# Kernel tuning notes

Measured on AMD Instinct MI355X. Metric: run time of the kernel, lower is better.

## Reference

```python
import jax, jax.numpy as jnp
import numpy as np

N, F, E, A, H = 50000, 64, 1600000, 8, 16
RECEPTIVE_FIELD = 7


def setup_inputs() -> dict:
    key = jax.random.key(0)
    ks = jax.random.split(key, 12)
    inp = {
        "x": jax.random.normal(ks[0], (N, F), dtype=jnp.float32),
        "edge_index": jax.random.randint(ks[1], (2, E), 0, N, dtype=jnp.int64),
        "w1": jax.random.normal(ks[2], (F, H), dtype=jnp.float32) * 0.1,
        "b1": jax.random.normal(ks[3], (H,), dtype=jnp.float32) * 0.1,
        "w2": jax.random.normal(ks[4], (H, H), dtype=jnp.float32) * 0.1,
        "b2": jax.random.normal(ks[5], (H,), dtype=jnp.float32) * 0.1,
        "w3": jax.random.normal(ks[6], (H, F), dtype=jnp.float32) * 0.1,
        "b3": jax.random.normal(ks[7], (F,), dtype=jnp.float32) * 0.1,
        "fc1_w": jax.random.normal(ks[8], ((1 + RECEPTIVE_FIELD) * F, F), dtype=jnp.float32) * 0.05,
        "fc1_b": jax.random.normal(ks[9], (F,), dtype=jnp.float32) * 0.05,
        "fc2_w": jax.random.normal(ks[10], (F, A), dtype=jnp.float32) * 0.1,
        "fc2_b": jax.random.normal(ks[11], (A,), dtype=jnp.float32) * 0.1,
    }
    return inp


def _mlp(x, w1, b1, w2, b2, w3, b3):
    h = jax.nn.relu(x @ w1 + b1)
    h = jax.nn.relu(h @ w2 + b2)
    return h @ w3 + b3


def _agg_mean(x, src, dst):
    # scatter-mean: mean of source-node features over incoming edges per target
    s = jax.ops.segment_sum(x[src], dst, num_segments=N)          # [N, F]
    cnt = jax.ops.segment_sum(jnp.ones((src.shape[0], 1), x.dtype), dst, num_segments=N)
    return s / jnp.maximum(cnt, 1.0)  # nodes with no in-edges -> 0 (torch mean aggr)


def reference(x, edge_index, w1, b1, w2, b2, w3, b3, fc1_w, fc1_b, fc2_w, fc2_b):
    src, dst = edge_index[0], edge_index[1]
    mlp = lambda t: _mlp(t, w1, b1, w2, b2, w3, b3)
    fields = [mlp(mlp(x))]
    for i in range(RECEPTIVE_FIELD):
        x_ = mlp(x)
        for _ in range(i + 1):
            x_ = _agg_mean(x_, src, dst)
        fields.append(mlp(x_))
    f = jnp.concatenate(fields, axis=1)          # [N, 8*F]
    h = f @ fc1_w + fc1_b                        # [N, F]
    logits = h @ fc2_w + fc2_b                   # [N, A]
    return jax.nn.softmax(logits, axis=-1)       # Categorical probs
```

## Files before the change

### kernel.cpp

```cpp
#include <hip/hip_runtime.h>
#include <hip/hip_fp16.h>


#define NB2MAX 400
#define NBLK   256
#define CAP2   32
#define CAPC   48
#define CAPB   6144
#define OVCAP  1024
#define LCAP   6144
#define CAPN   64

__global__ __launch_bounds__(1024) void binfill_k(
    const int* __restrict__ src, const int* __restrict__ dst, int E, int n,
    int* __restrict__ gcur, int* __restrict__ ovbuf,
    int* __restrict__ bins, int* __restrict__ cnts,
    const float* __restrict__ w1, const float* __restrict__ w3,
    const float* __restrict__ b3, const float* __restrict__ fc1w,
    const float* __restrict__ fc1b, const float* __restrict__ fc2w,
    const float* __restrict__ fc2b,
    float* __restrict__ M, float* __restrict__ cvec,
    float* __restrict__ W31, float* __restrict__ c31) {
    __shared__ int lbuf[NB2MAX * CAP2];
    __shared__ int lcnt[NB2MAX];
    __shared__ int lflush[NB2MAX];
    int tid = threadIdx.x;
    int NB = (n + 127) >> 7;

    if ((int)blockIdx.x >= NBLK) {
        float* fl = (float*)lbuf;
        int s = (int)blockIdx.x - NBLK;
        if (s == 0) {
            if (tid < 256) {
                int i = tid >> 4, j = tid & 15;
                float a = 0.f;
                for (int g = 0; g < 64; g++) a += w3[i * 64 + g] * w1[g * 16 + j];
                W31[tid] = a;
            } else if (tid < 272) {
                int j = tid - 256;
                float a = 0.f;
                for (int g = 0; g < 64; g++) a += b3[g] * w1[g * 16 + j];
                c31[j] = a;
            } else if (tid >= 320 && tid < 384) {
                int h = tid - 320;
                float a = 0.f;
                for (int r = 0; r < 512; r++) a += b3[r & 63] * fc1w[r * 64 + h];
                fl[h] = a;
            }
            __syncthreads();
            if (tid < 8) {
                float a = fc2b[tid];
                for (int h = 0; h < 64; h++) a += (fc1b[h] + fl[h]) * fc2w[h * 8 + tid];
                cvec[tid] = a;
            }
        } else {
            int k = s - 1;
            {
                int i = tid >> 6, h = tid & 63;
                float a = 0.f;
                const float* f1 = fc1w + (size_t)(k * 64) * 64 + h;
                for (int g = 0; g < 64; g++) a += w3[i * 64 + g] * f1[g * 64];
                fl[i * 64 + h] = a;
            }
            __syncthreads();
            if (tid < 128) {
                int i = tid >> 3, j = tid & 7;
                float a = 0.f;
                for (int h = 0; h < 64; h++) a += fl[i * 64 + h] * fc2w[h * 8 + j];
                M[k * 128 + i * 8 + j] = a;
            }
        }
        return;
    }

    for (int b = tid; b < NB; b += 1024) { lcnt[b] = 0; lflush[b] = 0; }
    __syncthreads();
    int blk = blockIdx.x;
    int chunk = (E + NBLK - 1) / NBLK;
    int beg = blk * chunk;
    int end = beg + chunk; if (end > E) end = E;
    for (int t0 = beg; t0 < end; t0 += 1024) {
        int e = t0 + tid;
        if (e < end) {
            int d = dst[e], s = src[e];
            if ((unsigned)d < (unsigned)n && (unsigned)s < (unsigned)n) {
                int b = d >> 7;
                int pk = ((d & 127) << 16) | s;
                int pos = atomicAdd(&lcnt[b], 1);
                if (pos < CAP2) lbuf[b * CAP2 + pos] = pk;
                else {
                    int p = atomicAdd(&gcur[b], 1);
                    if (p < OVCAP) ovbuf[b * OVCAP + p] = pk;
                }
            }
        }
        __syncthreads();
        for (int b = tid; b < NB; b += 1024) {
            int cnt = lcnt[b]; if (cnt > CAP2) cnt = CAP2;
            int fl2 = lflush[b];
            size_t cell = ((size_t)b * NBLK + blk) * CAPC;
            int base = 0;
            while (cnt - base >= 16) {
                if (fl2 + 16 <= CAPC) {
                    int* dp = bins + cell + fl2;
                    #pragma unroll
                    for (int q = 0; q < 16; q++) dp[q] = lbuf[b * CAP2 + base + q];
                    fl2 += 16;
                } else {
                    int p = atomicAdd(&gcur[b], 16);
                    for (int q = 0; q < 16; q++)
                        if (p + q < OVCAP) ovbuf[b * OVCAP + p + q] = lbuf[b * CAP2 + base + q];
                }
                base += 16;
            }
            int rem = cnt - base;
            if (base > 0)
                for (int q = 0; q < rem; q++) lbuf[b * CAP2 + q] = lbuf[b * CAP2 + base + q];
            lcnt[b] = rem; lflush[b] = fl2;
        }
        __syncthreads();
    }
    for (int b = tid; b < NB; b += 1024) {
        int cnt = lcnt[b]; if (cnt > CAP2) cnt = CAP2;
        int fl2 = lflush[b];
        size_t cell = ((size_t)b * NBLK + blk) * CAPC;
        if (fl2 + cnt <= CAPC) {
            for (int q = 0; q < cnt; q++) bins[cell + fl2 + q] = lbuf[b * CAP2 + q];
            fl2 += cnt;
        } else {
            int p = atomicAdd(&gcur[b], cnt);
            for (int q = 0; q < cnt; q++)
                if (p + q < OVCAP) ovbuf[b * OVCAP + p + q] = lbuf[b * CAP2 + q];
        }
        cnts[(size_t)blk * NB + b] = fl2;
    }
}

__global__ __launch_bounds__(256) void csr2_k(
    const int* __restrict__ bins, const int* __restrict__ cnts,
    const int* __restrict__ gcur, const int* __restrict__ ovbuf,
    unsigned short* __restrict__ csrp_s, int2* __restrict__ nd_s,
    int* __restrict__ csr, int2* __restrict__ be, int* __restrict__ lcnt3,
    int n) {
    __shared__ int hist[128], pref[128], cur[128], slot[128];
    __shared__ int scnt[NBLK];
    __shared__ int lbuf[LCAP];
    __shared__ int sov;
    __shared__ int ccnt[3], cbase[3];
    int tid = threadIdx.x;
    int NB = (n + 127) >> 7;
    int b = blockIdx.x;
    if (tid < 128) { hist[tid] = 0; cur[tid] = 0; }
    if (tid < 3) ccnt[tid] = 0;
    scnt[tid] = cnts[(size_t)tid * NB + b];
    if (tid == 0) {
        int g = gcur[b];
        sov = g < 0 ? 0 : (g > OVCAP ? OVCAP : g);
    }
    __syncthreads();
    {
        int c = scnt[tid];
        size_t cell = ((size_t)b * NBLK + tid) * CAPC;
        for (int i = 0; i < c; i++) atomicAdd(&hist[bins[cell + i] >> 16], 1);
    }
    if (tid == 0)
        for (int i = 0; i < sov; i++) atomicAdd(&hist[ovbuf[b * OVCAP + i] >> 16], 1);
    __syncthreads();
    if (tid == 0) {
        int r = 0;
        for (int i = 0; i < 128; i++) { pref[i] = r; r += hist[i]; }
    }
    __syncthreads();
    {
        int c = scnt[tid];
        size_t cell = ((size_t)b * NBLK + tid) * CAPC;
        for (int i = 0; i < c; i++) {
            int pk = bins[cell + i];
            int dl = pk >> 16;
            int pos = pref[dl] + atomicAdd(&cur[dl], 1);
            if (pos < LCAP) lbuf[pos] = pk & 0xffff;
        }
    }
    if (tid == 0) {
        for (int i = 0; i < sov; i++) {
            int pk = ovbuf[b * OVCAP + i];
            int dl = pk >> 16;
            int pos = pref[dl] + atomicAdd(&cur[dl], 1);
            if (pos < LCAP) lbuf[pos] = pk & 0xffff;
        }
    }
    __syncthreads();
    int myc = -1, lpos = 0;
    if (tid < 128) {
        int d = (b << 7) + tid;
        if (d < n) {
            int cnt = hist[tid];
            myc = cnt <= 32 ? 0 : (cnt <= 48 ? 1 : 2);
            lpos = atomicAdd(&ccnt[myc], 1);
        }
    }
    __syncthreads();
    if (tid < 3) cbase[tid] = atomicAdd(&lcnt3[tid], ccnt[tid]);
    __syncthreads();
    if (myc >= 0) {
        int d = (b << 7) + tid;
        int cnt = hist[tid];
        int s = myc * n + cbase[myc] + lpos;
        slot[tid] = s;
        nd_s[s] = make_int2(d, cnt);
        if (cnt > CAPN) {
            int s0 = b * CAPB + pref[tid];
            be[d] = make_int2(s0 + CAPN, s0 + cnt);
            for (int j = CAPN; j < cnt; j++)
                csr[s0 + j] = lbuf[pref[tid] + j] << 2;
        }
    }
    __syncthreads();
    for (int q = tid; q < 128 * CAPN; q += 256) {
        int dl = q >> 6, j = q & 63;
        int d = (b << 7) + dl;
        if (d >= n) break;
        int cnt = hist[dl];
        int v = (j < cnt) ? lbuf[pref[dl] + j] : n;
        int pos = ((j & 3) << 4) | (j >> 2);
        csrp_s[(size_t)slot[dl] * CAPN + pos] = (unsigned short)v;
    }
}

__device__ __forceinline__ void acc_row(uint2 u, float& ax, float& ay,
                                        float& az, float& aw) {
    __half2 p = *reinterpret_cast<const __half2*>(&u.x);
    __half2 q = *reinterpret_cast<const __half2*>(&u.y);
    float2 f = __half22float2(p), g = __half22float2(q);
    ax += f.x; ay += f.y; az += g.x; aw += g.y;
}

__global__ __launch_bounds__(256, 4) void proj_k(
    const float* __restrict__ x, __half* __restrict__ z0, __half* __restrict__ z1,
    float* __restrict__ logits,
    const float* __restrict__ w1, const float* __restrict__ b1,
    const float* __restrict__ w2, const float* __restrict__ b2,
    const float* __restrict__ W31, const float* __restrict__ c31,
    const float* __restrict__ M0, const float* __restrict__ cvec, int n) {
    __shared__ float sx[16 * 68];
    __shared__ float sw1[1024], sw2[256], sW[256], sM[128];
    __shared__ float sb1[16], sb2[16], sc[16], scv[8];
    int tid = threadIdx.x;
    for (int i = tid; i < 1024; i += 256) sw1[i] = w1[i];
    sw2[tid] = w2[tid];
    sW[tid] = W31[tid];
    if (tid < 128) sM[tid] = M0[tid];
    if (tid < 16) { sb1[tid] = b1[tid]; sb2[tid] = b2[tid]; sc[tid] = c31[tid]; }
    if (tid < 8) scv[tid] = cvec[tid];
    if (blockIdx.x == 0 && tid < 16) {
        ((unsigned short*)z0)[(size_t)n * 16 + tid] = 0;
        ((unsigned short*)z1)[(size_t)n * 16 + tid] = 0;
    }
    int node0 = blockIdx.x * 16;
    {
        int r = tid >> 4, c4 = tid & 15;
        if (node0 + r < n) {
            float4 v = ((const float4*)(x + (size_t)(node0 + r) * 64))[c4];
            float* dstp = sx + r * 68 + c4 * 4;
            dstp[0] = v.x; dstp[1] = v.y; dstp[2] = v.z; dstp[3] = v.w;
        }
    }
    __syncthreads();
    int nl = tid >> 4, jj = tid & 15;
    int node = node0 + nl;
    if (node >= n) return;
    float t1 = 0.f;
    const float* xr = sx + nl * 68;
    #pragma unroll
    for (int g = 0; g < 64; g++) t1 += xr[g] * sw1[g * 16 + jj];
    t1 = fmaxf(t1 + sb1[jj], 0.f);
    float t2 = sb2[jj];
    #pragma unroll
    for (int i = 0; i < 16; i++) t2 += __shfl(t1, i, 16) * sw2[i * 16 + jj];
    t2 = fmaxf(t2, 0.f);
    float zv = sc[jj];
    #pragma unroll
    for (int i = 0; i < 16; i++) zv += __shfl(t2, i, 16) * sW[i * 16 + jj];
    z0[(size_t)node * 16 + jj] = __float2half(zv);
    float hv = fmaxf(zv + sb1[jj], 0.f);
    float f2 = sb2[jj];
    #pragma unroll
    for (int i = 0; i < 16; i++) f2 += __shfl(hv, i, 16) * sw2[i * 16 + jj];
    f2 = fmaxf(f2, 0.f);
    float p0 = f2 * sM[jj * 8 + 0], p1 = f2 * sM[jj * 8 + 1];
    float p2 = f2 * sM[jj * 8 + 2], p3 = f2 * sM[jj * 8 + 3];
    float p4 = f2 * sM[jj * 8 + 4], p5 = f2 * sM[jj * 8 + 5];
    float p6 = f2 * sM[jj * 8 + 6], p7 = f2 * sM[jj * 8 + 7];
    #pragma unroll
    for (int off = 1; off < 16; off <<= 1) {
        p0 += __shfl_xor(p0, off, 16); p1 += __shfl_xor(p1, off, 16);
        p2 += __shfl_xor(p2, off, 16); p3 += __shfl_xor(p3, off, 16);
        p4 += __shfl_xor(p4, off, 16); p5 += __shfl_xor(p5, off, 16);
        p6 += __shfl_xor(p6, off, 16); p7 += __shfl_xor(p7, off, 16);
    }
    if (jj < 8) {
        float myp = jj == 0 ? p0 : jj == 1 ? p1 : jj == 2 ? p2 : jj == 3 ? p3
                  : jj == 4 ? p4 : jj == 5 ? p5 : jj == 6 ? p6 : p7;
        logits[(size_t)node * 8 + jj] = scv[jj] + myp;
    }
}

__global__ __launch_bounds__(256, 4) void hop_k(
    const __half* __restrict__ zin, __half* __restrict__ zout,
    float* __restrict__ logits,
    const unsigned short* __restrict__ csrp_s, const int2* __restrict__ nd_s,
    const int2* __restrict__ be, const int* __restrict__ csr,
    const int* __restrict__ lcnt3,
    const float* __restrict__ w2, const float* __restrict__ b1,
    const float* __restrict__ b2, const float* __restrict__ M, int n, int FB) {
    __shared__ float sw2[256], sM[128], sb1[16], sb2[16];
    int tid = threadIdx.x;
    if ((int)blockIdx.x < FB) {
        sw2[tid] = w2[tid];
        if (tid < 128) sM[tid] = M[tid];
        if (tid < 16) { sb1[tid] = b1[tid]; sb2[tid] = b2[tid]; }
        __syncthreads();
        int nid = blockIdx.x * 256 + tid;
        if (nid >= n) return;
        float h[16];
        const __half2* zp = (const __half2*)(zin + (size_t)nid * 16);
        #pragma unroll
        for (int q = 0; q < 8; q++) {
            float2 f = __half22float2(zp[q]);
            h[2 * q] = f.x; h[2 * q + 1] = f.y;
        }
        #pragma unroll
        for (int i = 0; i < 16; i++) h[i] = fmaxf(h[i] + sb1[i], 0.f);
        float t2[16];
        #pragma unroll
        for (int j = 0; j < 16; j++) {
            float a = sb2[j];
            #pragma unroll
            for (int i = 0; i < 16; i++) a += h[i] * sw2[i * 16 + j];
            t2[j] = fmaxf(a, 0.f);
        }
        float* lp = logits + (size_t)nid * 8;
        #pragma unroll
        for (int j = 0; j < 8; j++) {
            float l = 0.f;
            #pragma unroll
            for (int i = 0; i < 16; i++) l += t2[i] * sM[i * 8 + j];
            lp[j] += l;
        }
        return;
    }
    int wave = tid >> 6;
    int lane = tid & 63;
    int quarter = lane >> 4;
    int l16 = lane & 15;
    int t4 = l16 >> 2, ch = l16 & 3;
    int idx = (((int)blockIdx.x - FB) * 4 + wave) * 4 + quarter;
    if (idx >= n) return;
    int ns = lcnt3[0], nm = lcnt3[1];
    int tier; size_t row;
    if (idx < ns)           { tier = 0; row = (size_t)idx; }
    else if (idx < ns + nm) { tier = 1; row = (size_t)n + (idx - ns); }
    else                    { tier = 2; row = 2 * (size_t)n + (idx - ns - nm); }
    int2 nd = nd_s[row];
    int node = nd.x, degi = nd.y;
    const uint4* ip = (const uint4*)(csrp_s + (row << 6));
    uint4 pa = ip[t4 * 2];
    int r0 = pa.x & 0xffff, r1 = pa.x >> 16;
    int r2 = pa.y & 0xffff, r3 = pa.y >> 16;
    int r4 = pa.z & 0xffff, r5 = pa.z >> 16;
    int r6 = pa.w & 0xffff, r7 = pa.w >> 16;
    const uint2* z2 = (const uint2*)zin;
    uint2 u0 = z2[((size_t)r0 << 2) + ch];
    uint2 u1 = z2[((size_t)r1 << 2) + ch];
    uint2 u2 = z2[((size_t)r2 << 2) + ch];
    uint2 u3 = z2[((size_t)r3 << 2) + ch];
    uint2 u4 = z2[((size_t)r4 << 2) + ch];
    uint2 u5 = z2[((size_t)r5 << 2) + ch];
    uint2 u6 = z2[((size_t)r6 << 2) + ch];
    uint2 u7 = z2[((size_t)r7 << 2) + ch];
    float ax = 0.f, ay = 0.f, az = 0.f, aw = 0.f;
    acc_row(u0, ax, ay, az, aw); acc_row(u1, ax, ay, az, aw);
    acc_row(u2, ax, ay, az, aw); acc_row(u3, ax, ay, az, aw);
    acc_row(u4, ax, ay, az, aw); acc_row(u5, ax, ay, az, aw);
    acc_row(u6, ax, ay, az, aw); acc_row(u7, ax, ay, az, aw);
    if (tier >= 1) {
        uint4 pb = ip[t4 * 2 + 1];
        int r8 = pb.x & 0xffff, r9 = pb.x >> 16;
        int rA = pb.y & 0xffff, rB = pb.y >> 16;
        uint2 u8 = z2[((size_t)r8 << 2) + ch];
        uint2 u9 = z2[((size_t)r9 << 2) + ch];
        uint2 uA = z2[((size_t)rA << 2) + ch];
        uint2 uB = z2[((size_t)rB << 2) + ch];
        acc_row(u8, ax, ay, az, aw); acc_row(u9, ax, ay, az, aw);
        acc_row(uA, ax, ay, az, aw); acc_row(uB, ax, ay, az, aw);
        if (tier == 2) {
            int rC = pb.z & 0xffff, rD = pb.z >> 16;
            int rE = pb.w & 0xffff, rF = pb.w >> 16;
            uint2 uC = z2[((size_t)rC << 2) + ch];
            uint2 uD = z2[((size_t)rD << 2) + ch];
            uint2 uE = z2[((size_t)rE << 2) + ch];
            uint2 uF = z2[((size_t)rF << 2) + ch];
            acc_row(uC, ax, ay, az, aw); acc_row(uD, ax, ay, az, aw);
            acc_row(uE, ax, ay, az, aw); acc_row(uF, ax, ay, az, aw);
            if (degi > CAPN) {
                int2 r = be[node];
                for (int q = r.x + t4; q < r.y; q += 4) {
                    uint2 u = z2[(size_t)csr[q] + ch];
                    acc_row(u, ax, ay, az, aw);
                }
            }
        }
    }
    #pragma unroll
    for (int off = 8; off >= 4; off >>= 1) {
        ax += __shfl_down(ax, off, 16);
        ay += __shfl_down(ay, off, 16);
        az += __shfl_down(az, off, 16);
        aw += __shfl_down(aw, off, 16);
    }
    if (l16 < 4) {
        float inv = 1.f / (float)(degi > 0 ? degi : 1);
        __half2 h01 = __floats2half2_rn(ax * inv, ay * inv);
        __half2 h23 = __floats2half2_rn(az * inv, aw * inv);
        uint2 w;
        w.x = *reinterpret_cast<unsigned int*>(&h01);
        w.y = *reinterpret_cast<unsigned int*>(&h23);
        ((uint2*)(zout + (size_t)node * 16))[l16] = w;
    }
}

__global__ __launch_bounds__(256) void fieldsoft_k(
    const __half* __restrict__ z, float* __restrict__ logits,
    const float* __restrict__ w2, const float* __restrict__ b1,
    const float* __restrict__ b2, const float* __restrict__ M, int n) {
    __shared__ float sw2[256], sM[128], sb1[16], sb2[16];
    int tid = threadIdx.x;
    sw2[tid] = w2[tid];
    if (tid < 128) sM[tid] = M[tid];
    if (tid < 16) { sb1[tid] = b1[tid]; sb2[tid] = b2[tid]; }
    __syncthreads();
    int nid = blockIdx.x * 256 + tid;
    if (nid >= n) return;
    float h[16];
    const __half2* zp = (const __half2*)(z + (size_t)nid * 16);
    #pragma unroll
    for (int q = 0; q < 8; q++) {
        float2 f = __half22float2(zp[q]);
        h[2 * q] = f.x; h[2 * q + 1] = f.y;
    }
    #pragma unroll
    for (int i = 0; i < 16; i++) h[i] = fmaxf(h[i] + sb1[i], 0.f);
    float t2[16];
    #pragma unroll
    for (int j = 0; j < 16; j++) {
        float a = sb2[j];
        #pragma unroll
        for (int i = 0; i < 16; i++) a += h[i] * sw2[i * 16 + j];
        t2[j] = fmaxf(a, 0.f);
    }
    float4* lp4 = (float4*)(logits + (size_t)nid * 8);
    float4 l0 = lp4[0], l1 = lp4[1];
    float v[8] = {l0.x, l0.y, l0.z, l0.w, l1.x, l1.y, l1.z, l1.w};
    #pragma unroll
    for (int j = 0; j < 8; j++) {
        float l = 0.f;
        #pragma unroll
        for (int i = 0; i < 16; i++) l += t2[i] * sM[i * 8 + j];
        v[j] += l;
    }
    float m = v[0];
    #pragma unroll
    for (int j = 1; j < 8; j++) m = fmaxf(m, v[j]);
    float s = 0.f;
    #pragma unroll
    for (int j = 0; j < 8; j++) { v[j] = expf(v[j] - m); s += v[j]; }
    float inv = 1.f / s;
    lp4[0] = make_float4(v[0] * inv, v[1] * inv, v[2] * inv, v[3] * inv);
    lp4[1] = make_float4(v[4] * inv, v[5] * inv, v[6] * inv, v[7] * inv);
}

extern "C" void kernel_launch(void* const* d_in, const int* in_sizes, int n_in,
                              void* d_out, int out_size, void* d_ws, size_t ws_size,
                              hipStream_t stream) {
    const float* x    = (const float*)d_in[0];
    const int*   ei   = (const int*)d_in[1];
    const float* w1   = (const float*)d_in[2];
    const float* b1   = (const float*)d_in[3];
    const float* w2   = (const float*)d_in[4];
    const float* b2   = (const float*)d_in[5];
    const float* w3   = (const float*)d_in[6];
    const float* b3   = (const float*)d_in[7];
    const float* fc1w = (const float*)d_in[8];
    const float* fc1b = (const float*)d_in[9];
    const float* fc2w = (const float*)d_in[10];
    const float* fc2b = (const float*)d_in[11];
    float* out = (float*)d_out;

    int n = in_sizes[0] / 64;
    int E = in_sizes[1] / 2;
    int NB = (n + 127) >> 7;
    const int* src = ei;
    const int* dst = ei + E;

    char* ws = (char*)d_ws;
    auto carve = [&](size_t bytes) {
        char* p = ws;
        ws += (bytes + 255) & ~((size_t)255);
        return p;
    };
    int*   gcur    = (int*)carve((size_t)NB * 4);
    int*   lcnt3   = (int*)carve(16);
    int*   ovbuf   = (int*)carve((size_t)NB * OVCAP * 4);
    int*   binsbuf = (int*)carve((size_t)NB * NBLK * CAPC * 4);
    int*   cnts    = (int*)carve((size_t)NBLK * NB * 4);
    unsigned short* csrp_s = (unsigned short*)carve((size_t)3 * n * CAPN * 2);
    int2*  nd_s    = (int2*)carve((size_t)3 * n * 8);
    int*   csr     = (int*)carve((size_t)NB * CAPB * 4);
    int2*  be      = (int2*)carve((size_t)n * 8);
    __half* buf0   = (__half*)carve((size_t)(n + 1) * 16 * 2);
    __half* buf1   = (__half*)carve((size_t)(n + 1) * 16 * 2);
    float* M       = (float*)carve(1024 * 4);
    float* cvec    = (float*)carve(8 * 4);
    float* W31     = (float*)carve(256 * 4);
    float* c31     = (float*)carve(16 * 4);

    size_t gpad = ((size_t)NB * 4 + 255) & ~((size_t)255);
    hipMemsetAsync(gcur, 0, gpad + 16, stream);
    binfill_k<<<NBLK + 9, 1024, 0, stream>>>(src, dst, E, n, gcur, ovbuf, binsbuf, cnts,
                                             w1, w3, b3, fc1w, fc1b, fc2w, fc2b,
                                             M, cvec, W31, c31);
    csr2_k<<<NB, 256, 0, stream>>>(binsbuf, cnts, gcur, ovbuf,
                                   csrp_s, nd_s, csr, be, lcnt3, n);

    int FB  = (n + 255) / 256;
    int FBJ = (n + 15) / 16;
    int AB  = (n + 15) / 16;
    proj_k<<<FBJ, 256, 0, stream>>>(x, buf0, buf1, out, w1, b1, w2, b2,
                                    W31, c31, M, cvec, n);

    __half* cur = buf0;
    __half* nxt = buf1;
    hop_k<<<AB, 256, 0, stream>>>(cur, nxt, out, csrp_s, nd_s, be, csr, lcnt3,
                                  w2, b1, b2, M, n, 0);
    { __half* t = cur; cur = nxt; nxt = t; }
    for (int k = 1; k <= 6; k++) {
        hop_k<<<FB + AB, 256, 0, stream>>>(cur, nxt, out, csrp_s, nd_s, be, csr,
                                           lcnt3, w2, b1, b2, M + k * 128, n, FB);
        __half* t = cur; cur = nxt; nxt = t;
    }
    fieldsoft_k<<<FB, 256, 0, stream>>>(cur, out, w2, b1, b2, M + 7 * 128, n);
}
```

Before: 243.2 us.

## Merge CSR build and projection into one launch; parallelize final field/softmax per feature

The CSR construction kernel and the node projection kernel are independent, so they are merged into one launch. The first NB blocks build the CSR and the remaining blocks run the projection, with shared memory overlaid through a union. This removes a launch boundary and lets the two stages run concurrently. The final field+softmax kernel now maps 16 threads per node with shuffle reductions instead of one thread per node, which raises parallelism and cuts per-thread register pressure. The cost is a larger union smem footprint for projection blocks, which may lower their occupancy.

```diff
diff --git a/kernel.cpp b/kernel.cpp
--- a/kernel.cpp
+++ b/kernel.cpp
@@ -136,94 +136,173 @@
     }
 }
 
-__global__ __launch_bounds__(256) void csr2_k(
+struct SmemC {
+    int hist[128], pref[128], cur[128], slot[128];
+    int scnt[NBLK];
+    int lbuf[LCAP];
+    int sov;
+    int ccnt[3], cbase[3];
+};
+struct SmemP {
+    float sx[16 * 68];
+    float sw1[1024], sw2[256], sW[256], sM[128];
+    float sb1[16], sb2[16], sc[16], scv[8];
+};
+union SmemU { SmemC c; SmemP p; };
+
+__global__ __launch_bounds__(256) void csr2proj_k(
     const int* __restrict__ bins, const int* __restrict__ cnts,
     const int* __restrict__ gcur, const int* __restrict__ ovbuf,
     unsigned short* __restrict__ csrp_s, int2* __restrict__ nd_s,
     int* __restrict__ csr, int2* __restrict__ be, int* __restrict__ lcnt3,
-    int n) {
-    __shared__ int hist[128], pref[128], cur[128], slot[128];
-    __shared__ int scnt[NBLK];
-    __shared__ int lbuf[LCAP];
-    __shared__ int sov;
-    __shared__ int ccnt[3], cbase[3];
+    const float* __restrict__ x, __half* __restrict__ z0, __half* __restrict__ z1,
+    float* __restrict__ logits,
+    const float* __restrict__ w1, const float* __restrict__ b1,
+    const float* __restrict__ w2, const float* __restrict__ b2,
+    const float* __restrict__ W31, const float* __restrict__ c31,
+    const float* __restrict__ M0, const float* __restrict__ cvec,
+    int n, int NBARG) {
+    __shared__ SmemU smem;
     int tid = threadIdx.x;
-    int NB = (n + 127) >> 7;
-    int b = blockIdx.x;
-    if (tid < 128) { hist[tid] = 0; cur[tid] = 0; }
-    if (tid < 3) ccnt[tid] = 0;
-    scnt[tid] = cnts[(size_t)tid * NB + b];
-    if (tid == 0) {
-        int g = gcur[b];
-        sov = g < 0 ? 0 : (g > OVCAP ? OVCAP : g);
+    if ((int)blockIdx.x < NBARG) {
+        SmemC& sc_ = smem.c;
+        int NB = NBARG;
+        int b = blockIdx.x;
+        if (tid < 128) { sc_.hist[tid] = 0; sc_.cur[tid] = 0; }
+        if (tid < 3) sc_.ccnt[tid] = 0;
+        sc_.scnt[tid] = cnts[(size_t)tid * NB + b];
+        if (tid == 0) {
+            int g = gcur[b];
+            sc_.sov = g < 0 ? 0 : (g > OVCAP ? OVCAP : g);
+        }
+        __syncthreads();
+        {
+            int c = sc_.scnt[tid];
+            size_t cell = ((size_t)b * NBLK + tid) * CAPC;
+            for (int i = 0; i < c; i++) atomicAdd(&sc_.hist[bins[cell + i] >> 16], 1);
+        }
+        if (tid == 0)
+            for (int i = 0; i < sc_.sov; i++)
+                atomicAdd(&sc_.hist[ovbuf[b * OVCAP + i] >> 16], 1);
+        __syncthreads();
+        if (tid == 0) {
+            int r = 0;
+            for (int i = 0; i < 128; i++) { sc_.pref[i] = r; r += sc_.hist[i]; }
+        }
+        __syncthreads();
+        {
+            int c = sc_.scnt[tid];
+            size_t cell = ((size_t)b * NBLK + tid) * CAPC;
+            for (int i = 0; i < c; i++) {
+                int pk = bins[cell + i];
+                int dl = pk >> 16;
+                int pos = sc_.pref[dl] + atomicAdd(&sc_.cur[dl], 1);
+                if (pos < LCAP) sc_.lbuf[pos] = pk & 0xffff;
+            }
+        }
+        if (tid == 0) {
+            for (int i = 0; i < sc_.sov; i++) {
+                int pk = ovbuf[b * OVCAP + i];
+                int dl = pk >> 16;
+                int pos = sc_.pref[dl] + atomicAdd(&sc_.cur[dl], 1);
+                if (pos < LCAP) sc_.lbuf[pos] = pk & 0xffff;
+            }
+        }
+        __syncthreads();
+        int myc = -1, lpos = 0;
+        if (tid < 128) {
+            int d = (b << 7) + tid;
+            if (d < n) {
+                int cnt = sc_.hist[tid];
+                myc = cnt <= 32 ? 0 : (cnt <= 48 ? 1 : 2);
+                lpos = atomicAdd(&sc_.ccnt[myc], 1);
+            }
+        }
+        __syncthreads();
+        if (tid < 3) sc_.cbase[tid] = atomicAdd(&lcnt3[tid], sc_.ccnt[tid]);
+        __syncthreads();
+        if (myc >= 0) {
+            int d = (b << 7) + tid;
+            int cnt = sc_.hist[tid];
+            int s = myc * n + sc_.cbase[myc] + lpos;
+            sc_.slot[tid] = s;
+            nd_s[s] = make_int2(d, cnt);
+            if (cnt > CAPN) {
+                int s0 = b * CAPB + sc_.pref[tid];
+                be[d] = make_int2(s0 + CAPN, s0 + cnt);
+                for (int j = CAPN; j < cnt; j++)
+                    csr[s0 + j] = sc_.lbuf[sc_.pref[tid] + j] << 2;
+            }
+        }
+        __syncthreads();
+        for (int q = tid; q < 128 * CAPN; q += 256) {
+            int dl = q >> 6, j = q & 63;
+            int d = (b << 7) + dl;
+            if (d >= n) break;
+            int cnt = sc_.hist[dl];
+            int v = (j < cnt) ? sc_.lbuf[sc_.pref[dl] + j] : n;
+            int pos = ((j & 3) << 4) | (j >> 2);
+            csrp_s[(size_t)sc_.slot[dl] * CAPN + pos] = (unsigned short)v;
+        }
+        return;
+    }
+    SmemP& sp = smem.p;
+    for (int i = tid; i < 1024; i += 256) sp.sw1[i] = w1[i];
+    sp.sw2[tid] = w2[tid];
+    sp.sW[tid] = W31[tid];
+    if (tid < 128) sp.sM[tid] = M0[tid];
+    if (tid < 16) { sp.sb1[tid] = b1[tid]; sp.sb2[tid] = b2[tid]; sp.sc[tid] = c31[tid]; }
+    if (tid < 8) sp.scv[tid] = cvec[tid];
+    if ((int)blockIdx.x == NBARG && tid < 16) {
+        ((unsigned short*)z0)[(size_t)n * 16 + tid] = 0;
+        ((unsigned short*)z1)[(size_t)n * 16 + tid] = 0;
+    }
+    int node0 = ((int)blockIdx.x - NBARG) * 16;
+    {
+        int r = tid >> 4, c4 = tid & 15;
+        if (node0 + r < n) {
+            float4 v = ((const float4*)(x + (size_t)(node0 + r) * 64))[c4];
+            float* dstp = sp.sx + r * 68 + c4 * 4;
+            dstp[0] = v.x; dstp[1] = v.y; dstp[2] = v.z; dstp[3] = v.w;
+        }
     }
     __syncthreads();
-    {
-        int c = scnt[tid];
-        size_t cell = ((size_t)b * NBLK + tid) * CAPC;
-        for (int i = 0; i < c; i++) atomicAdd(&hist[bins[cell + i] >> 16], 1);
-    }
-    if (tid == 0)
-        for (int i = 0; i < sov; i++) atomicAdd(&hist[ovbuf[b * OVCAP + i] >> 16], 1);
-    __syncthreads();
-    if (tid == 0) {
-        int r = 0;
-        for (int i = 0; i < 128; i++) { pref[i] = r; r += hist[i]; }
-    }
-    __syncthreads();
-    {
-        int c = scnt[tid];
-        size_t cell = ((size_t)b * NBLK + tid) * CAPC;
-        for (int i = 0; i < c; i++) {
-            int pk = bins[cell + i];
-            int dl = pk >> 16;
-            int pos = pref[dl] + atomicAdd(&cur[dl], 1);
-            if (pos < LCAP) lbuf[pos] = pk & 0xffff;
-        }
-    }
-    if (tid == 0) {
-        for (int i = 0; i < sov; i++) {
-            int pk = ovbuf[b * OVCAP + i];
-            int dl = pk >> 16;
-            int pos = pref[dl] + atomicAdd(&cur[dl], 1);
-            if (pos < LCAP) lbuf[pos] = pk & 0xffff;
-        }
-    }
-    __syncthreads();
-    int myc = -1, lpos = 0;
-    if (tid < 128) {
-        int d = (b << 7) + tid;
-        if (d < n) {
-            int cnt = hist[tid];
-            myc = cnt <= 32 ? 0 : (cnt <= 48 ? 1 : 2);
-            lpos = atomicAdd(&ccnt[myc], 1);
-        }
-    }
-    __syncthreads();
-    if (tid < 3) cbase[tid] = atomicAdd(&lcnt3[tid], ccnt[tid]);
-    __syncthreads();
-    if (myc >= 0) {
-        int d = (b << 7) + tid;
-        int cnt = hist[tid];
-        int s = myc * n + cbase[myc] + lpos;
-        slot[tid] = s;
-        nd_s[s] = make_int2(d, cnt);
-        if (cnt > CAPN) {
-            int s0 = b * CAPB + pref[tid];
-            be[d] = make_int2(s0 + CAPN, s0 + cnt);
-            for (int j = CAPN; j < cnt; j++)
-                csr[s0 + j] = lbuf[pref[tid] + j] << 2;
-        }
-    }
-    __syncthreads();
-    for (int q = tid; q < 128 * CAPN; q += 256) {
-        int dl = q >> 6, j = q & 63;
-        int d = (b << 7) + dl;
-        if (d >= n) break;
-        int cnt = hist[dl];
-        int v = (j < cnt) ? lbuf[pref[dl] + j] : n;
-        int pos = ((j & 3) << 4) | (j >> 2);
-        csrp_s[(size_t)slot[dl] * CAPN + pos] = (unsigned short)v;
+    int nl = tid >> 4, jj = tid & 15;
+    int node = node0 + nl;
+    if (node >= n) return;
+    float t1 = 0.f;
+    const float* xr = sp.sx + nl * 68;
+    #pragma unroll
+    for (int g = 0; g < 64; g++) t1 += xr[g] * sp.sw1[g * 16 + jj];
+    t1 = fmaxf(t1 + sp.sb1[jj], 0.f);
+    float t2 = sp.sb2[jj];
+    #pragma unroll
+    for (int i = 0; i < 16; i++) t2 += __shfl(t1, i, 16) * sp.sw2[i * 16 + jj];
+    t2 = fmaxf(t2, 0.f);
+    float zv = sp.sc[jj];
+    #pragma unroll
+    for (int i = 0; i < 16; i++) zv += __shfl(t2, i, 16) * sp.sW[i * 16 + jj];
+    z0[(size_t)node * 16 + jj] = __float2half(zv);
+    float hv = fmaxf(zv + sp.sb1[jj], 0.f);
+    float f2 = sp.sb2[jj];
+    #pragma unroll
+    for (int i = 0; i < 16; i++) f2 += __shfl(hv, i, 16) * sp.sw2[i * 16 + jj];
+    f2 = fmaxf(f2, 0.f);
+    float p0 = f2 * sp.sM[jj * 8 + 0], p1 = f2 * sp.sM[jj * 8 + 1];
+    float p2 = f2 * sp.sM[jj * 8 + 2], p3 = f2 * sp.sM[jj * 8 + 3];
+    float p4 = f2 * sp.sM[jj * 8 + 4], p5 = f2 * sp.sM[jj * 8 + 5];
+    float p6 = f2 * sp.sM[jj * 8 + 6], p7 = f2 * sp.sM[jj * 8 + 7];
+    #pragma unroll
+    for (int off = 1; off < 16; off <<= 1) {
+        p0 += __shfl_xor(p0, off, 16); p1 += __shfl_xor(p1, off, 16);
+        p2 += __shfl_xor(p2, off, 16); p3 += __shfl_xor(p3, off, 16);
+        p4 += __shfl_xor(p4, off, 16); p5 += __shfl_xor(p5, off, 16);
+        p6 += __shfl_xor(p6, off, 16); p7 += __shfl_xor(p7, off, 16);
+    }
+    if (jj < 8) {
+        float myp = jj == 0 ? p0 : jj == 1 ? p1 : jj == 2 ? p2 : jj == 3 ? p3
+                  : jj == 4 ? p4 : jj == 5 ? p5 : jj == 6 ? p6 : p7;
+        logits[(size_t)node * 8 + jj] = sp.scv[jj] + myp;
     }
 }
 
@@ -233,76 +312,6 @@
     __half2 q = *reinterpret_cast<const __half2*>(&u.y);
     float2 f = __half22float2(p), g = __half22float2(q);
     ax += f.x; ay += f.y; az += g.x; aw += g.y;
-}
-
-__global__ __launch_bounds__(256, 4) void proj_k(
-    const float* __restrict__ x, __half* __restrict__ z0, __half* __restrict__ z1,
-    float* __restrict__ logits,
-    const float* __restrict__ w1, const float* __restrict__ b1,
-    const float* __restrict__ w2, const float* __restrict__ b2,
-    const float* __restrict__ W31, const float* __restrict__ c31,
-    const float* __restrict__ M0, const float* __restrict__ cvec, int n) {
-    __shared__ float sx[16 * 68];
-    __shared__ float sw1[1024], sw2[256], sW[256], sM[128];
-    __shared__ float sb1[16], sb2[16], sc[16], scv[8];
-    int tid = threadIdx.x;
-    for (int i = tid; i < 1024; i += 256) sw1[i] = w1[i];
-    sw2[tid] = w2[tid];
-    sW[tid] = W31[tid];
-    if (tid < 128) sM[tid] = M0[tid];
-    if (tid < 16) { sb1[tid] = b1[tid]; sb2[tid] = b2[tid]; sc[tid] = c31[tid]; }
-    if (tid < 8) scv[tid] = cvec[tid];
-    if (blockIdx.x == 0 && tid < 16) {
-        ((unsigned short*)z0)[(size_t)n * 16 + tid] = 0;
-        ((unsigned short*)z1)[(size_t)n * 16 + tid] = 0;
-    }
-    int node0 = blockIdx.x * 16;
-    {
-        int r = tid >> 4, c4 = tid & 15;
-        if (node0 + r < n) {
-            float4 v = ((const float4*)(x + (size_t)(node0 + r) * 64))[c4];
-            float* dstp = sx + r * 68 + c4 * 4;
-            dstp[0] = v.x; dstp[1] = v.y; dstp[2] = v.z; dstp[3] = v.w;
-        }
-    }
-    __syncthreads();
-    int nl = tid >> 4, jj = tid & 15;
-    int node = node0 + nl;
-    if (node >= n) return;
-    float t1 = 0.f;
-    const float* xr = sx + nl * 68;
-    #pragma unroll
-    for (int g = 0; g < 64; g++) t1 += xr[g] * sw1[g * 16 + jj];
-    t1 = fmaxf(t1 + sb1[jj], 0.f);
-    float t2 = sb2[jj];
-    #pragma unroll
-    for (int i = 0; i < 16; i++) t2 += __shfl(t1, i, 16) * sw2[i * 16 + jj];
-    t2 = fmaxf(t2, 0.f);
-    float zv = sc[jj];
-    #pragma unroll
-    for (int i = 0; i < 16; i++) zv += __shfl(t2, i, 16) * sW[i * 16 + jj];
-    z0[(size_t)node * 16 + jj] = __float2half(zv);
-    float hv = fmaxf(zv + sb1[jj], 0.f);
-    float f2 = sb2[jj];
-    #pragma unroll
-    for (int i = 0; i < 16; i++) f2 += __shfl(hv, i, 16) * sw2[i * 16 + jj];
-    f2 = fmaxf(f2, 0.f);
-    float p0 = f2 * sM[jj * 8 + 0], p1 = f2 * sM[jj * 8 + 1];
-    float p2 = f2 * sM[jj * 8 + 2], p3 = f2 * sM[jj * 8 + 3];
-    float p4 = f2 * sM[jj * 8 + 4], p5 = f2 * sM[jj * 8 + 5];
-    float p6 = f2 * sM[jj * 8 + 6], p7 = f2 * sM[jj * 8 + 7];
-    #pragma unroll
-    for (int off = 1; off < 16; off <<= 1) {
-        p0 += __shfl_xor(p0, off, 16); p1 += __shfl_xor(p1, off, 16);
-        p2 += __shfl_xor(p2, off, 16); p3 += __shfl_xor(p3, off, 16);
-        p4 += __shfl_xor(p4, off, 16); p5 += __shfl_xor(p5, off, 16);
-        p6 += __shfl_xor(p6, off, 16); p7 += __shfl_xor(p7, off, 16);
-    }
-    if (jj < 8) {
-        float myp = jj == 0 ? p0 : jj == 1 ? p1 : jj == 2 ? p2 : jj == 3 ? p3
-                  : jj == 4 ? p4 : jj == 5 ? p5 : jj == 6 ? p6 : p7;
-        logits[(size_t)node * 8 + jj] = scv[jj] + myp;
-    }
 }
 
 __global__ __launch_bounds__(256, 4) void hop_k(
@@ -429,7 +438,7 @@
     }
 }
 
-__global__ __launch_bounds__(256) void fieldsoft_k(
+__global__ __launch_bounds__(256, 4) void fieldsoft_k(
     const __half* __restrict__ z, float* __restrict__ logits,
     const float* __restrict__ w2, const float* __restrict__ b1,
     const float* __restrict__ b2, const float* __restrict__ M, int n) {
@@ -439,44 +448,40 @@
     if (tid < 128) sM[tid] = M[tid];
     if (tid < 16) { sb1[tid] = b1[tid]; sb2[tid] = b2[tid]; }
     __syncthreads();
-    int nid = blockIdx.x * 256 + tid;
-    if (nid >= n) return;
-    float h[16];
-    const __half2* zp = (const __half2*)(z + (size_t)nid * 16);
-    #pragma unroll
-    for (int q = 0; q < 8; q++) {
-        float2 f = __half22float2(zp[q]);
-        h[2 * q] = f.x; h[2 * q + 1] = f.y;
-    }
-    #pragma unroll
-    for (int i = 0; i < 16; i++) h[i] = fmaxf(h[i] + sb1[i], 0.f);
-    float t2[16];
-    #pragma unroll
-    for (int j = 0; j < 16; j++) {
-        float a = sb2[j];
-        #pragma unroll
-        for (int i = 0; i < 16; i++) a += h[i] * sw2[i * 16 + j];
-        t2[j] = fmaxf(a, 0.f);
-    }
-    float4* lp4 = (float4*)(logits + (size_t)nid * 8);
-    float4 l0 = lp4[0], l1 = lp4[1];
-    float v[8] = {l0.x, l0.y, l0.z, l0.w, l1.x, l1.y, l1.z, l1.w};
-    #pragma unroll
-    for (int j = 0; j < 8; j++) {
-        float l = 0.f;
-        #pragma unroll
-        for (int i = 0; i < 16; i++) l += t2[i] * sM[i * 8 + j];
-        v[j] += l;
-    }
-    float m = v[0];
-    #pragma unroll
-    for (int j = 1; j < 8; j++) m = fmaxf(m, v[j]);
-    float s = 0.f;
-    #pragma unroll
-    for (int j = 0; j < 8; j++) { v[j] = expf(v[j] - m); s += v[j]; }
-    float inv = 1.f / s;
-    lp4[0] = make_float4(v[0] * inv, v[1] * inv, v[2] * inv, v[3] * inv);
-    lp4[1] = make_float4(v[4] * inv, v[5] * inv, v[6] * inv, v[7] * inv);
+    int nl = tid >> 4, jj = tid & 15;
+    int node = blockIdx.x * 16 + nl;
+    if (node >= n) return;
+    float zv = __half2float(z[(size_t)node * 16 + jj]);
+    float hv = fmaxf(zv + sb1[jj], 0.f);
+    float t2 = sb2[jj];
+    #pragma unroll
+    for (int i = 0; i < 16; i++) t2 += __shfl(hv, i, 16) * sw2[i * 16 + jj];
+    t2 = fmaxf(t2, 0.f);
+    float p0 = t2 * sM[jj * 8 + 0], p1 = t2 * sM[jj * 8 + 1];
+    float p2 = t2 * sM[jj * 8 + 2], p3 = t2 * sM[jj * 8 + 3];
+    float p4 = t2 * sM[jj * 8 + 4], p5 = t2 * sM[jj * 8 + 5];
+    float p6 = t2 * sM[jj * 8 + 6], p7 = t2 * sM[jj * 8 + 7];
+    #pragma unroll
+    for (int off = 1; off < 16; off <<= 1) {
+        p0 += __shfl_xor(p0, off, 16); p1 += __shfl_xor(p1, off, 16);
+        p2 += __shfl_xor(p2, off, 16); p3 += __shfl_xor(p3, off, 16);
+        p4 += __shfl_xor(p4, off, 16); p5 += __shfl_xor(p5, off, 16);
+        p6 += __shfl_xor(p6, off, 16); p7 += __shfl_xor(p7, off, 16);
+    }
+    int q = jj & 7;
+    float myp = q == 0 ? p0 : q == 1 ? p1 : q == 2 ? p2 : q == 3 ? p3
+              : q == 4 ? p4 : q == 5 ? p5 : q == 6 ? p6 : p7;
+    float lg = myp + logits[(size_t)node * 8 + q];
+    float m = lg;
+    m = fmaxf(m, __shfl_xor(m, 1, 8));
+    m = fmaxf(m, __shfl_xor(m, 2, 8));
+    m = fmaxf(m, __shfl_xor(m, 4, 8));
+    float e = expf(lg - m);
+    float s = e;
+    s += __shfl_xor(s, 1, 8);
+    s += __shfl_xor(s, 2, 8);
+    s += __shfl_xor(s, 4, 8);
+    if (jj < 8) logits[(size_t)node * 8 + jj] = e / s;
 }
 
 extern "C" void kernel_launch(void* const* d_in, const int* in_sizes, int n_in,
@@ -529,14 +534,14 @@
     binfill_k<<<NBLK + 9, 1024, 0, stream>>>(src, dst, E, n, gcur, ovbuf, binsbuf, cnts,
                                              w1, w3, b3, fc1w, fc1b, fc2w, fc2b,
                                              M, cvec, W31, c31);
-    csr2_k<<<NB, 256, 0, stream>>>(binsbuf, cnts, gcur, ovbuf,
-                                   csrp_s, nd_s, csr, be, lcnt3, n);
 
     int FB  = (n + 255) / 256;
     int FBJ = (n + 15) / 16;
     int AB  = (n + 15) / 16;
-    proj_k<<<FBJ, 256, 0, stream>>>(x, buf0, buf1, out, w1, b1, w2, b2,
-                                    W31, c31, M, cvec, n);
+    csr2proj_k<<<NB + FBJ, 256, 0, stream>>>(binsbuf, cnts, gcur, ovbuf,
+                                             csrp_s, nd_s, csr, be, lcnt3,
+                                             x, buf0, buf1, out, w1, b1, w2, b2,
+                                             W31, c31, M, cvec, n, NB);
 
     __half* cur = buf0;
     __half* nxt = buf1;
@@ -548,5 +553,5 @@
                                            lcnt3, w2, b1, b2, M + k * 128, n, FB);
         __half* t = cur; cur = nxt; nxt = t;
     }
-    fieldsoft_k<<<FB, 256, 0, stream>>>(cur, out, w2, b1, b2, M + 7 * 128, n);
+    fieldsoft_k<<<FBJ, 256, 0, stream>>>(cur, out, w2, b1, b2, M + 7 * 128, n);
 }
```

Result: faster. 235.6 us, median of 3 (-3.1%).
